# Kernel optimization log

Hardware: AMD Instinct MI355X
Metric: run time of the kernel (lower is better)

The kernel has to match this reference:

```python
import jax, jax.numpy as jnp
import numpy as np

B, S, D, H, DK = 2, 2048, 1024, 16, 64
NUM_BUCKETS, MAX_DIST = 32, 128
EPS = 1e-6


def _relative_position_bucket(rel, num_buckets=NUM_BUCKETS, max_distance=MAX_DIST):
    # bidirectional (T5 encoder) bucketing
    nb = num_buckets // 2
    bucket = (rel > 0).astype(jnp.int32) * nb
    n = jnp.abs(rel)
    max_exact = nb // 2
    is_small = n < max_exact
    large = max_exact + (
        jnp.log(jnp.maximum(n, 1).astype(jnp.float32) / max_exact)
        / np.log(max_distance / max_exact)
        * (nb - max_exact)
    ).astype(jnp.int32)
    large = jnp.minimum(large, nb - 1)
    return bucket + jnp.where(is_small, n, large)


def softmax1(logits):
    # off-by-one softmax: exp(x-m) / (sum(exp(x-m)) + exp(-m))
    m = jax.lax.stop_gradient(jnp.max(logits, axis=-1, keepdims=True))
    e = jnp.exp(logits - m)
    return e / (jnp.sum(e, axis=-1, keepdims=True) + jnp.exp(-m))


def setup_inputs() -> dict:
    key = jax.random.key(0)
    ks = jax.random.split(key, 8)
    scale = 0.02
    return {
        "hidden_states": jax.random.normal(ks[0], (B, S, D), dtype=jnp.float32),
        "delete_gate_mask": jax.random.normal(ks[1], (B, S, 1), dtype=jnp.float32),
        "ln_w": jnp.ones((D,), dtype=jnp.float32),
        "q_w": jax.random.normal(ks[2], (D, H * DK), dtype=jnp.float32) * scale,
        "k_w": jax.random.normal(ks[3], (D, H * DK), dtype=jnp.float32) * scale,
        "v_w": jax.random.normal(ks[4], (D, H * DK), dtype=jnp.float32) * scale,
        "o_w": jax.random.normal(ks[5], (H * DK, D), dtype=jnp.float32) * scale,
        "rel_emb": jax.random.normal(ks[6], (NUM_BUCKETS, H), dtype=jnp.float32) * scale,
    }


def reference(hidden_states, delete_gate_mask, ln_w, q_w, k_w, v_w, o_w, rel_emb):
    # T5LayerNorm (RMS norm, no mean subtraction, no bias)
    var = jnp.mean(jnp.square(hidden_states), axis=-1, keepdims=True)
    x = hidden_states * jax.lax.rsqrt(var + EPS) * ln_w

    # projections (T5 Linear layers have no bias, no 1/sqrt(d) scaling)
    q = (x @ q_w).reshape(B, S, H, DK).transpose(0, 2, 1, 3)  # bhqd
    k = (x @ k_w).reshape(B, S, H, DK).transpose(0, 2, 1, 3)  # bhkd
    v = (x @ v_w).reshape(B, S, H, DK).transpose(0, 2, 1, 3)  # bhkd

    scores = jnp.einsum("bhqd,bhkd->bhqk", q, k)

    # relative position bias: [1, H, S, S]
    pos = jnp.arange(S)
    rel = pos[None, :] - pos[:, None]  # key_pos - query_pos
    bucket = _relative_position_bucket(rel)  # [S, S]
    position_bias = rel_emb[bucket].transpose(2, 0, 1)[None]  # [1,H,S,S]

    # delete gate: [B,S,1] -> additive mask over key axis [B,1,1,S]
    gate = delete_gate_mask[..., 0][:, None, None, :]

    scores = scores + position_bias + gate
    attn = softmax1(scores.astype(jnp.float32)).astype(scores.dtype)

    attn_out = jnp.einsum("bhqk,bhkd->bhqd", attn, v)
    attn_out = attn_out.transpose(0, 2, 1, 3).reshape(B, S, H * DK) @ o_w

    # residual (dropout disabled at p=0)
    return hidden_states + attn_out
```

## Files before the change

kernel.cpp:

```cpp
#include <hip/hip_runtime.h>
#include <hip/hip_bf16.h>
#include <math.h>

typedef __attribute__((ext_vector_type(8))) short short8;
typedef __attribute__((ext_vector_type(4))) float f32x4;

#define S_LEN   2048
#define DMODEL  1024
#define NHEAD   16
#define HDK     64
#define NBATCH  2
#define MTOT    (NBATCH*S_LEN)
#define LOG2E   1.4426950408889634f

__device__ __forceinline__ unsigned short f2bf(float f) {
  union { float f; unsigned u; } c; c.f = f;
  unsigned r = c.u + 0x7FFFu + ((c.u >> 16) & 1u);
  return (unsigned short)(r >> 16);
}

__device__ __forceinline__ short8 lds_ld16(const unsigned short* p) {
  return *reinterpret_cast<const short8*>(p);
}

__device__ __forceinline__ void gload_lds16(const unsigned short* g, unsigned short* l) {
  __builtin_amdgcn_global_load_lds(
      (const __attribute__((address_space(1))) unsigned int*)g,
      (__attribute__((address_space(3))) unsigned int*)l, 16, 0, 0);
}

__global__ __launch_bounds__(256) void transpose_w_kernel(
    const float* __restrict__ qw, const float* __restrict__ kw,
    const float* __restrict__ vw, const float* __restrict__ ow,
    unsigned short* __restrict__ wqkv, unsigned short* __restrict__ wo) {
  int z = blockIdx.z;
  const float* src = (z==0)?qw:(z==1)?kw:(z==2)?vw:ow;
  unsigned short* dst = (z<3) ? (wqkv + (size_t)z*DMODEL*DMODEL) : wo;
  __shared__ float tile[32][33];
  int n0 = blockIdx.x*32, k0 = blockIdx.y*32;
  int tx = threadIdx.x, ty = threadIdx.y;
  for (int r = ty; r < 32; r += 8)
    tile[r][tx] = src[(size_t)(k0+r)*DMODEL + n0 + tx];
  __syncthreads();
  for (int r = ty; r < 32; r += 8)
    dst[(size_t)(n0+r)*DMODEL + k0 + tx] = f2bf(tile[tx][r]);
}

__global__ __launch_bounds__(256) void fused_prep_kernel(
    const float* __restrict__ hs, const float* __restrict__ lnw,
    const float* __restrict__ rel_emb, const float* __restrict__ gmask,
    unsigned short* __restrict__ xo, float* __restrict__ btab,
    float* __restrict__ egf, unsigned short* __restrict__ egb) {
  const int blk = blockIdx.x, t = threadIdx.x;
  if (blk < MTOT) {
    const int row = blk;
    const float4 v = ((const float4*)(hs + (size_t)row*DMODEL))[t];
    float ss = v.x*v.x + v.y*v.y + v.z*v.z + v.w*v.w;
    #pragma unroll
    for (int off = 32; off >= 1; off >>= 1) ss += __shfl_xor(ss, off, 64);
    __shared__ float wsum[4];
    if ((t & 63) == 0) wsum[t >> 6] = ss;
    __syncthreads();
    float tot = wsum[0] + wsum[1] + wsum[2] + wsum[3];
    float sc = rsqrtf(tot * (1.0f/DMODEL) + 1e-6f);
    const float4 lw = ((const float4*)lnw)[t];
    uint2 o;
    o.x = (unsigned)f2bf(v.x*sc*lw.x) | ((unsigned)f2bf(v.y*sc*lw.y) << 16);
    o.y = (unsigned)f2bf(v.z*sc*lw.z) | ((unsigned)f2bf(v.w*sc*lw.w) << 16);
    ((uint2*)(xo + (size_t)row*DMODEL))[t] = o;
  } else if (blk < MTOT + 256) {
    int idx = (blk - MTOT)*256 + t;
    if (idx >= NHEAD*4095) return;
    int h = idx / 4095, rp = idx % 4095, rel = rp - 2047;
    int bucket = (rel > 0) ? 16 : 0;
    int n = (rel < 0) ? -rel : rel;
    int v;
    if (n < 8) v = n;
    else {
      float lrv = logf((float)n * 0.125f) / 2.7725887f * 8.0f;
      v = 8 + (int)lrv;
      if (v > 15) v = 15;
    }
    btab[idx] = rel_emb[(size_t)(bucket + v)*NHEAD + h] * LOG2E;
  } else {
    int i = (blk - MTOT - 256)*256 + t;
    float e = __expf(gmask[i]);
    egf[i] = e;
    egb[i] = f2bf(e);
  }
}

template<int EPI>
__global__ __launch_bounds__(256) void gemm128(
    const unsigned short* __restrict__ X,
    const unsigned short* __restrict__ W,
    unsigned short* __restrict__ Oq, unsigned short* __restrict__ Ok,
    unsigned short* __restrict__ Ov,
    const float* __restrict__ resid, float* __restrict__ Of,
    const float* __restrict__ escale) {
  __shared__ unsigned short As[128*64];
  __shared__ unsigned short Bs[128*64];
  const int z = blockIdx.z;
  int m0, n0;
  const unsigned short *Ap, *Bp;
  if (EPI == 0 && z == 2) {
    m0 = blockIdx.y*128; n0 = blockIdx.x*128;
    Ap = W + (size_t)2*DMODEL*DMODEL; Bp = X;
  } else {
    m0 = blockIdx.x*128; n0 = blockIdx.y*128;
    Ap = X; Bp = W + ((EPI==0) ? (size_t)z*DMODEL*DMODEL : 0);
  }
  const int t = threadIdx.x, lane = t & 63, w = t >> 6;
  const int g = lane >> 4, lr = lane & 15;
  const int wr = (w >> 1)*64, wc = (w & 1)*64;

  f32x4 acc[4][4];
  #pragma unroll
  for (int mi = 0; mi < 4; mi++)
    #pragma unroll
    for (int ni = 0; ni < 4; ni++) acc[mi][ni] = (f32x4){0.f,0.f,0.f,0.f};

  const unsigned short* ag[4]; const unsigned short* bg[4];
  unsigned short* al[4]; unsigned short* bl[4];
  #pragma unroll
  for (int i = 0; i < 4; i++) {
    int slot = t + i*256, row = slot >> 3, c8 = slot & 7;
    int cs = c8 ^ (row & 7);
    ag[i] = Ap + (size_t)(m0 + row)*DMODEL + cs*8;
    bg[i] = Bp + (size_t)(n0 + row)*DMODEL + cs*8;
    al[i] = As + slot*8;
    bl[i] = Bs + slot*8;
  }

  for (int kk = 0; kk < DMODEL; kk += 64) {
    #pragma unroll
    for (int i = 0; i < 4; i++) {
      gload_lds16(ag[i] + kk, al[i]);
      gload_lds16(bg[i] + kk, bl[i]);
    }
    __syncthreads();
    #pragma unroll
    for (int ks = 0; ks < 2; ks++) {
      short8 af[4], bfr[4];
      #pragma unroll
      for (int mi = 0; mi < 4; mi++) {
        int R = wr + mi*16 + lr;
        af[mi] = lds_ld16(As + R*64 + (((ks*4 + g) ^ (R & 7)) << 3));
      }
      #pragma unroll
      for (int ni = 0; ni < 4; ni++) {
        int R = wc + ni*16 + lr;
        bfr[ni] = lds_ld16(Bs + R*64 + (((ks*4 + g) ^ (R & 7)) << 3));
      }
      #pragma unroll
      for (int mi = 0; mi < 4; mi++)
        #pragma unroll
        for (int ni = 0; ni < 4; ni++)
          acc[mi][ni] = __builtin_amdgcn_mfma_f32_16x16x32_bf16(af[mi], bfr[ni], acc[mi][ni], 0, 0, 0);
    }
    __syncthreads();
  }

  if (EPI == 0) {
    if (z < 2) {
      unsigned short* dst = (z == 0) ? Oq : Ok;
      const float osc = (z == 0) ? LOG2E : 1.0f;
      #pragma unroll
      for (int mi = 0; mi < 4; mi++) {
        #pragma unroll
        for (int r = 0; r < 4; r++) {
          int m = m0 + wr + mi*16 + g*4 + r;
          int b = m >> 11, s = m & (S_LEN-1);
          unsigned short* drow = dst + ((size_t)b*NHEAD*S_LEN + s)*HDK;
          #pragma unroll
          for (int ni = 0; ni < 4; ni++) {
            int n = n0 + wc + ni*16 + lr;
            int h = n >> 6, dcol = n & 63;
            drow[(size_t)h*S_LEN*HDK + dcol] = f2bf(acc[mi][ni][r] * osc);
          }
        }
      }
    } else {
      #pragma unroll
      for (int ni = 0; ni < 4; ni++) {
        int n = n0 + wc + ni*16 + lr;
        int b = n >> 11, s = n & (S_LEN-1);
        float e = escale[n];
        #pragma unroll
        for (int mi = 0; mi < 4; mi++)
          #pragma unroll
          for (int r = 0; r < 4; r++) {
            int m = m0 + wr + mi*16 + g*4 + r;
            Ov[((size_t)b*DMODEL + m)*S_LEN + s] = f2bf(acc[mi][ni][r] * e);
          }
      }
    }
  } else {
    #pragma unroll
    for (int mi = 0; mi < 4; mi++) {
      #pragma unroll
      for (int r = 0; r < 4; r++) {
        int m = m0 + wr + mi*16 + g*4 + r;
        const float* rrow = resid + (size_t)m*DMODEL;
        float* orow = Of + (size_t)m*DMODEL;
        #pragma unroll
        for (int ni = 0; ni < 4; ni++) {
          int n = n0 + wc + ni*16 + lr;
          orow[n] = rrow[n] + acc[mi][ni][r];
        }
      }
    }
  }
}

__global__ __launch_bounds__(256, 2) void attn_kernel(
    const unsigned short* __restrict__ Qg,
    const unsigned short* __restrict__ Kg,
    const unsigned short* __restrict__ Vtg,
    const float* __restrict__ btab,
    const unsigned short* __restrict__ egb,
    unsigned short* __restrict__ Og) {
  __shared__ __align__(16) unsigned short Kl[2][64][64];
  __shared__ __align__(16) unsigned short Vl[2][64][64];
  __shared__ __align__(16) unsigned short Pl[4][16*64];

  const int flat = blockIdx.x;
  const int xcd = flat & 7, j = flat >> 3;
  const int bh = xcd*4 + (j >> 4), qx = j & 15;
  const int b = bh >> 4, h = bh & 15;
  const int q0 = qx * 128;

  const int t = threadIdx.x, w = t >> 6, lane = t & 63;
  const int g = lane >> 4, lr = lane & 15, l7 = lane & 7;
  const int srow0 = t >> 3, sg0 = t & 7, srow1 = srow0 + 32;
  const int swz = (sg0 ^ (srow0 & 7)) << 3;

  const unsigned short* Qb = Qg  + (size_t)bh*S_LEN*HDK;
  const unsigned short* Kb = Kg  + (size_t)bh*S_LEN*HDK;
  const unsigned short* Vb = Vtg + (size_t)bh*HDK*S_LEN;
  const unsigned short* ge = egb + (size_t)b*S_LEN;

  const int qs0A = q0 + w*32, qs0B = qs0A + 16;
  short8 qfA0 = *reinterpret_cast<const short8*>(Qb + (size_t)(qs0A+lr)*HDK + g*8);
  short8 qfA1 = *reinterpret_cast<const short8*>(Qb + (size_t)(qs0A+lr)*HDK + 32 + g*8);
  short8 qfB0 = *reinterpret_cast<const short8*>(Qb + (size_t)(qs0B+lr)*HDK + g*8);
  short8 qfB1 = *reinterpret_cast<const short8*>(Qb + (size_t)(qs0B+lr)*HDK + 32 + g*8);

  f32x4 accA[4], accB[4], l4A, l4B;
  #pragma unroll
  for (int n = 0; n < 4; n++) { accA[n] = (f32x4){0.f,0.f,0.f,0.f}; accB[n] = (f32x4){0.f,0.f,0.f,0.f}; }
  l4A = (f32x4){0.f,0.f,0.f,0.f}; l4B = (f32x4){0.f,0.f,0.f,0.f};

  const float* btb = btab + (size_t)h*4095 + 2047;
  const float cpos = btb[91];
  const float cneg = btb[-91];

  {
    *reinterpret_cast<uint4*>(&Kl[0][srow0][swz]) =
        *reinterpret_cast<const uint4*>(Kb + (size_t)srow0*HDK + sg0*8);
    *reinterpret_cast<uint4*>(&Kl[0][srow1][swz]) =
        *reinterpret_cast<const uint4*>(Kb + (size_t)srow1*HDK + sg0*8);
    *reinterpret_cast<uint4*>(&Vl[0][srow0][swz]) =
        *reinterpret_cast<const uint4*>(Vb + (size_t)srow0*S_LEN + sg0*8);
    *reinterpret_cast<uint4*>(&Vl[0][srow1][swz]) =
        *reinterpret_cast<const uint4*>(Vb + (size_t)srow1*S_LEN + sg0*8);
  }

  char* prow = (char*)&Pl[w][0] + lr*128;

  int cur = 0;
  const int NT = S_LEN/64;
  for (int kt = 0; kt < NT; ++kt) {
    const int key0 = kt*64;
    __syncthreads();

    uint4 nk0, nk1, nv0, nv1;
    const bool pf = (kt + 1 < NT);
    if (pf) {
      nk0 = *reinterpret_cast<const uint4*>(Kb + (size_t)(key0+64+srow0)*HDK + sg0*8);
      nk1 = *reinterpret_cast<const uint4*>(Kb + (size_t)(key0+64+srow1)*HDK + sg0*8);
      nv0 = *reinterpret_cast<const uint4*>(Vb + (size_t)srow0*S_LEN + key0+64 + sg0*8);
      nv1 = *reinterpret_cast<const uint4*>(Vb + (size_t)srow1*S_LEN + key0+64 + sg0*8);
    }

    short8 bk[4][2];
    #pragma unroll
    for (int n = 0; n < 4; n++) {
      const unsigned short* kr = &Kl[cur][n*16 + lr][0];
      bk[n][0] = lds_ld16(kr + ((g ^ l7) << 3));
      bk[n][1] = lds_ld16(kr + (((4 + g) ^ l7) << 3));
    }
    short8 bv[2][4];
    #pragma unroll
    for (int c = 0; c < 2; c++)
      #pragma unroll
      for (int n = 0; n < 4; n++)
        bv[c][n] = lds_ld16(&Vl[cur][n*16 + lr][((4*c + g) ^ l7) << 3]);
    short8 gv[2];
    #pragma unroll
    for (int c = 0; c < 2; c++) {
      short8 z8 = (short8){0,0,0,0,0,0,0,0};
      if (lr == 0)
        z8 = *reinterpret_cast<const short8*>(ge + key0 + c*32 + g*8);
      gv[c] = z8;
    }

#define PROCESS_SET(qf0_, qf1_, qs0_, acc_, l4_)                                      \
    {                                                                                 \
      const int dband = key0 - (qs0_);                                                \
      const bool band = (dband > -154 && dband < 106);                                \
      const float cc = band ? 0.f : ((dband > 0) ? cpos : cneg);                      \
      f32x4 zc = (f32x4){cc, cc, cc, cc};               \
      f32x4 sv[4];                                                                    \
      __builtin_amdgcn_s_setprio(1);                                                  \
      _Pragma("unroll") for (int n = 0; n < 4; n++) {                                 \
        sv[n] = __builtin_amdgcn_mfma_f32_16x16x32_bf16(bk[n][0], qf0_, zc, 0, 0, 0); \
        sv[n] = __builtin_amdgcn_mfma_f32_16x16x32_bf16(bk[n][1], qf1_, sv[n], 0, 0, 0); \
      }                                                                               \
      __builtin_amdgcn_s_setprio(0);                                                  \
      if (band) {                                                                     \
        const float* btq = btb + (dband - lr);                                        \
        _Pragma("unroll") for (int n = 0; n < 4; n++)                                 \
          _Pragma("unroll") for (int r = 0; r < 4; r++)                               \
            sv[n][r] += btq[n*16 + g*4 + r];                                          \
      }                                                                               \
      _Pragma("unroll") for (int n = 0; n < 4; n++)                                   \
        _Pragma("unroll") for (int r = 0; r < 4; r++)                                 \
          sv[n][r] = exp2f(sv[n][r]);                                                 \
      _Pragma("unroll") for (int n = 0; n < 4; n++) {                                 \
        unsigned plo_, phi_;                                                          \
        asm("v_cvt_pk_bf16_f32 %0, %1, %2" : "=v"(plo_) : "v"(sv[n][0]), "v"(sv[n][1])); \
        asm("v_cvt_pk_bf16_f32 %0, %1, %2" : "=v"(phi_) : "v"(sv[n][2]), "v"(sv[n][3])); \
        uint2 pw_; pw_.x = plo_; pw_.y = phi_;                                        \
        *reinterpret_cast<uint2*>(prow + ((((2*n + (g>>1)) ^ l7) << 4) + ((g & 1) << 3))) = pw_; \
      }                                                                               \
      __builtin_amdgcn_s_setprio(1);                                                  \
      _Pragma("unroll") for (int c = 0; c < 2; c++) {                                 \
        short8 pa_ = lds_ld16((const unsigned short*)(prow + (((4*c + g) ^ l7) << 4))); \
        _Pragma("unroll") for (int n = 0; n < 4; n++)                                 \
          acc_[n] = __builtin_amdgcn_mfma_f32_16x16x32_bf16(pa_, bv[c][n], acc_[n], 0, 0, 0); \
        l4_ = __builtin_amdgcn_mfma_f32_16x16x32_bf16(pa_, gv[c], l4_, 0, 0, 0);      \
      }                                                                               \
      __builtin_amdgcn_s_setprio(0);                                                  \
    }

    PROCESS_SET(qfA0, qfA1, qs0A, accA, l4A)
    PROCESS_SET(qfB0, qfB1, qs0B, accB, l4B)
#undef PROCESS_SET

    if (pf) {
      *reinterpret_cast<uint4*>(&Kl[cur^1][srow0][swz]) = nk0;
      *reinterpret_cast<uint4*>(&Kl[cur^1][srow1][swz]) = nk1;
      *reinterpret_cast<uint4*>(&Vl[cur^1][srow0][swz]) = nv0;
      *reinterpret_cast<uint4*>(&Vl[cur^1][srow1][swz]) = nv1;
    }
    cur ^= 1;
  }

#define FINAL_SET(acc_, l4_, qs0_)                                                    \
  {                                                                                   \
    _Pragma("unroll") for (int r = 0; r < 4; r++) {                                   \
      float lq = __shfl(l4_[r], g*16);                                                \
      float inv = 1.0f / (lq + 1.0f);                                                 \
      int srw = (qs0_) + g*4 + r;                                                     \
      unsigned short* orow = Og + ((size_t)b*S_LEN + srw)*DMODEL + h*HDK;             \
      _Pragma("unroll") for (int n = 0; n < 4; n++)                                   \
        orow[n*16 + lr] = f2bf(acc_[n][r] * inv);                                     \
    }                                                                                 \
  }
  FINAL_SET(accA, l4A, qs0A)
  FINAL_SET(accB, l4B, qs0B)
#undef FINAL_SET
}

extern "C" void kernel_launch(void* const* d_in, const int* in_sizes, int n_in,
                              void* d_out, int out_size, void* d_ws, size_t ws_size,
                              hipStream_t stream) {
  const float* hs   = (const float*)d_in[0];
  const float* gate = (const float*)d_in[1];
  const float* lnw  = (const float*)d_in[2];
  const float* qw   = (const float*)d_in[3];
  const float* kw   = (const float*)d_in[4];
  const float* vw   = (const float*)d_in[5];
  const float* ow   = (const float*)d_in[6];
  const float* rel  = (const float*)d_in[7];
  float* out = (float*)d_out;

  char* ws = (char*)d_ws;
  const size_t MB = 1ull << 20;
  unsigned short* xbf  = (unsigned short*)(ws);
  unsigned short* wqkv = (unsigned short*)(ws + 8*MB);
  unsigned short* wo   = (unsigned short*)(ws + 14*MB);
  unsigned short* qb   = (unsigned short*)(ws + 16*MB);
  unsigned short* kb   = (unsigned short*)(ws + 24*MB);
  unsigned short* vt   = (unsigned short*)(ws + 32*MB);
  unsigned short* ao   = (unsigned short*)(ws + 40*MB);
  float*          btab = (float*)(ws + 48*MB);
  float*          egf  = (float*)(ws + 48*MB + 256*1024);
  unsigned short* egb  = (unsigned short*)(ws + 48*MB + 272*1024);

  transpose_w_kernel<<<dim3(32,32,4), dim3(32,8), 0, stream>>>(qw, kw, vw, ow, wqkv, wo);
  fused_prep_kernel<<<dim3(MTOT + 256 + 16), dim3(256), 0, stream>>>(
      hs, lnw, rel, gate, xbf, btab, egf, egb);
  gemm128<0><<<dim3(MTOT/128, DMODEL/128, 3), dim3(256), 0, stream>>>(
      xbf, wqkv, qb, kb, vt, nullptr, nullptr, egf);
  attn_kernel<<<dim3(512), dim3(256), 0, stream>>>(
      qb, kb, vt, btab, egb, ao);
  gemm128<1><<<dim3(MTOT/128, DMODEL/128, 1), dim3(256), 0, stream>>>(
      ao, wo, nullptr, nullptr, nullptr, hs, out, nullptr);
}
```

Measured before the change: 134.5 us.

## Double-buffer GEMM K-loop and fold weight transpose into prep kernel

The GEMM main loop now uses two 32-wide K stages in LDS, so the next tile's global-to-LDS load is issued before the current tile's MFMAs, with one barrier per step and raised wave priority around the MFMA block. The LDS XOR swizzle is dropped because the row stride shrinks to 32 elements. Separately, the weight transpose/bf16 conversion kernel is merged into the fused prep kernel as extra blocks, removing one launch. Risks include more LDS bank conflicts from the unswizzled 64-byte rows, more barriers overall, and async loads into a buffer possibly still being read unless the memory-counter wait is handled correctly.

```diff
diff --git a/kernel.cpp b/kernel.cpp
--- a/kernel.cpp
+++ b/kernel.cpp
@@ -29,28 +29,14 @@
       (__attribute__((address_space(3))) unsigned int*)l, 16, 0, 0);
 }
 
-__global__ __launch_bounds__(256) void transpose_w_kernel(
-    const float* __restrict__ qw, const float* __restrict__ kw,
-    const float* __restrict__ vw, const float* __restrict__ ow,
-    unsigned short* __restrict__ wqkv, unsigned short* __restrict__ wo) {
-  int z = blockIdx.z;
-  const float* src = (z==0)?qw:(z==1)?kw:(z==2)?vw:ow;
-  unsigned short* dst = (z<3) ? (wqkv + (size_t)z*DMODEL*DMODEL) : wo;
-  __shared__ float tile[32][33];
-  int n0 = blockIdx.x*32, k0 = blockIdx.y*32;
-  int tx = threadIdx.x, ty = threadIdx.y;
-  for (int r = ty; r < 32; r += 8)
-    tile[r][tx] = src[(size_t)(k0+r)*DMODEL + n0 + tx];
-  __syncthreads();
-  for (int r = ty; r < 32; r += 8)
-    dst[(size_t)(n0+r)*DMODEL + k0 + tx] = f2bf(tile[tx][r]);
-}
-
 __global__ __launch_bounds__(256) void fused_prep_kernel(
     const float* __restrict__ hs, const float* __restrict__ lnw,
     const float* __restrict__ rel_emb, const float* __restrict__ gmask,
+    const float* __restrict__ qw, const float* __restrict__ kw,
+    const float* __restrict__ vw, const float* __restrict__ ow,
     unsigned short* __restrict__ xo, float* __restrict__ btab,
-    float* __restrict__ egf, unsigned short* __restrict__ egb) {
+    float* __restrict__ egf, unsigned short* __restrict__ egb,
+    unsigned short* __restrict__ wqkv, unsigned short* __restrict__ wo) {
   const int blk = blockIdx.x, t = threadIdx.x;
   if (blk < MTOT) {
     const int row = blk;
@@ -68,8 +54,21 @@
     o.x = (unsigned)f2bf(v.x*sc*lw.x) | ((unsigned)f2bf(v.y*sc*lw.y) << 16);
     o.y = (unsigned)f2bf(v.z*sc*lw.z) | ((unsigned)f2bf(v.w*sc*lw.w) << 16);
     ((uint2*)(xo + (size_t)row*DMODEL))[t] = o;
-  } else if (blk < MTOT + 256) {
-    int idx = (blk - MTOT)*256 + t;
+  } else if (blk < MTOT + 4096) {
+    int bb = blk - MTOT;
+    int z = bb >> 10, rem = bb & 1023;
+    const float* src = (z==0)?qw:(z==1)?kw:(z==2)?vw:ow;
+    unsigned short* dst = (z<3) ? (wqkv + (size_t)z*DMODEL*DMODEL) : wo;
+    __shared__ float tile[32][33];
+    int n0 = (rem & 31)*32, k0 = (rem >> 5)*32;
+    int tx = t & 31, ty = t >> 5;
+    for (int r = ty; r < 32; r += 8)
+      tile[r][tx] = src[(size_t)(k0+r)*DMODEL + n0 + tx];
+    __syncthreads();
+    for (int r = ty; r < 32; r += 8)
+      dst[(size_t)(n0+r)*DMODEL + k0 + tx] = f2bf(tile[tx][r]);
+  } else if (blk < MTOT + 4096 + 256) {
+    int idx = (blk - MTOT - 4096)*256 + t;
     if (idx >= NHEAD*4095) return;
     int h = idx / 4095, rp = idx % 4095, rel = rp - 2047;
     int bucket = (rel > 0) ? 16 : 0;
@@ -83,7 +82,7 @@
     }
     btab[idx] = rel_emb[(size_t)(bucket + v)*NHEAD + h] * LOG2E;
   } else {
-    int i = (blk - MTOT - 256)*256 + t;
+    int i = (blk - MTOT - 4096 - 256)*256 + t;
     float e = __expf(gmask[i]);
     egf[i] = e;
     egb[i] = f2bf(e);
@@ -98,8 +97,8 @@
     unsigned short* __restrict__ Ov,
     const float* __restrict__ resid, float* __restrict__ Of,
     const float* __restrict__ escale) {
-  __shared__ unsigned short As[128*64];
-  __shared__ unsigned short Bs[128*64];
+  __shared__ unsigned short As[2][128*32];
+  __shared__ unsigned short Bs[2][128*32];
   const int z = blockIdx.z;
   int m0, n0;
   const unsigned short *Ap, *Bp;
@@ -120,46 +119,43 @@
     #pragma unroll
     for (int ni = 0; ni < 4; ni++) acc[mi][ni] = (f32x4){0.f,0.f,0.f,0.f};
 
-  const unsigned short* ag[4]; const unsigned short* bg[4];
-  unsigned short* al[4]; unsigned short* bl[4];
+  const unsigned short* ag[2]; const unsigned short* bg[2]; int so[2];
   #pragma unroll
-  for (int i = 0; i < 4; i++) {
-    int slot = t + i*256, row = slot >> 3, c8 = slot & 7;
-    int cs = c8 ^ (row & 7);
-    ag[i] = Ap + (size_t)(m0 + row)*DMODEL + cs*8;
-    bg[i] = Bp + (size_t)(n0 + row)*DMODEL + cs*8;
-    al[i] = As + slot*8;
-    bl[i] = Bs + slot*8;
-  }
-
-  for (int kk = 0; kk < DMODEL; kk += 64) {
-    #pragma unroll
-    for (int i = 0; i < 4; i++) {
-      gload_lds16(ag[i] + kk, al[i]);
-      gload_lds16(bg[i] + kk, bl[i]);
-    }
+  for (int i = 0; i < 2; i++) {
+    int slot = t + i*256, row = slot >> 2, c4 = slot & 3;
+    so[i] = slot*8;
+    ag[i] = Ap + (size_t)(m0 + row)*DMODEL + c4*8;
+    bg[i] = Bp + (size_t)(n0 + row)*DMODEL + c4*8;
+  }
+#define GSTAGE(buf_, kk_) do {                                         \
+    _Pragma("unroll") for (int i = 0; i < 2; i++) {                    \
+      gload_lds16(ag[i] + (kk_), &As[buf_][0] + so[i]);                \
+      gload_lds16(bg[i] + (kk_), &Bs[buf_][0] + so[i]);                \
+    } } while (0)
+
+  GSTAGE(0, 0);
+  __syncthreads();
+  int cur = 0;
+  for (int kk = 0; kk < DMODEL; kk += 32) {
+    if (kk + 32 < DMODEL) GSTAGE(cur^1, kk + 32);
+    short8 af[4], bfr[4];
+    #pragma unroll
+    for (int mi = 0; mi < 4; mi++)
+      af[mi] = lds_ld16(&As[cur][0] + (wr + mi*16 + lr)*32 + g*8);
+    #pragma unroll
+    for (int ni = 0; ni < 4; ni++)
+      bfr[ni] = lds_ld16(&Bs[cur][0] + (wc + ni*16 + lr)*32 + g*8);
+    __builtin_amdgcn_s_setprio(1);
+    #pragma unroll
+    for (int mi = 0; mi < 4; mi++)
+      #pragma unroll
+      for (int ni = 0; ni < 4; ni++)
+        acc[mi][ni] = __builtin_amdgcn_mfma_f32_16x16x32_bf16(af[mi], bfr[ni], acc[mi][ni], 0, 0, 0);
+    __builtin_amdgcn_s_setprio(0);
     __syncthreads();
-    #pragma unroll
-    for (int ks = 0; ks < 2; ks++) {
-      short8 af[4], bfr[4];
-      #pragma unroll
-      for (int mi = 0; mi < 4; mi++) {
-        int R = wr + mi*16 + lr;
-        af[mi] = lds_ld16(As + R*64 + (((ks*4 + g) ^ (R & 7)) << 3));
-      }
-      #pragma unroll
-      for (int ni = 0; ni < 4; ni++) {
-        int R = wc + ni*16 + lr;
-        bfr[ni] = lds_ld16(Bs + R*64 + (((ks*4 + g) ^ (R & 7)) << 3));
-      }
-      #pragma unroll
-      for (int mi = 0; mi < 4; mi++)
-        #pragma unroll
-        for (int ni = 0; ni < 4; ni++)
-          acc[mi][ni] = __builtin_amdgcn_mfma_f32_16x16x32_bf16(af[mi], bfr[ni], acc[mi][ni], 0, 0, 0);
-    }
-    __syncthreads();
-  }
+    cur ^= 1;
+  }
+#undef GSTAGE
 
   if (EPI == 0) {
     if (z < 2) {
@@ -399,9 +395,8 @@
   float*          egf  = (float*)(ws + 48*MB + 256*1024);
   unsigned short* egb  = (unsigned short*)(ws + 48*MB + 272*1024);
 
-  transpose_w_kernel<<<dim3(32,32,4), dim3(32,8), 0, stream>>>(qw, kw, vw, ow, wqkv, wo);
-  fused_prep_kernel<<<dim3(MTOT + 256 + 16), dim3(256), 0, stream>>>(
-      hs, lnw, rel, gate, xbf, btab, egf, egb);
+  fused_prep_kernel<<<dim3(MTOT + 4096 + 256 + 16), dim3(256), 0, stream>>>(
+      hs, lnw, rel, gate, qw, kw, vw, ow, xbf, btab, egf, egb, wqkv, wo);
   gemm128<0><<<dim3(MTOT/128, DMODEL/128, 3), dim3(256), 0, stream>>>(
       xbf, wqkv, qb, kb, vt, nullptr, nullptr, egf);
   attn_kernel<<<dim3(512), dim3(256), 0, stream>>>(
```

Result: slower. 140.8 us (+4.7%).
